# Kernel tuning notes

Measured on AMD Instinct MI355X. Metric: run time of the kernel, lower is better.

Reference implementation:

```python
import jax, jax.numpy as jnp
import numpy as np

N, E = 50000, 800000
NFEAT, NHID, NCLASS = 512, 256, 64
RRELU_SLOPE = (1.0 / 8.0 + 1.0 / 3.0) / 2.0  # nn.RReLU eval-mode negative slope


def spmm(row, col, val, X):
    # sparse adj (COO: row, col, val) @ dense X -> [N, F]
    return jax.ops.segment_sum(X[col] * val[:, None], row, num_segments=N)


def setup_inputs() -> dict:
    key = jax.random.key(0)
    ks = jax.random.split(key, 12)
    x = jax.random.normal(ks[0], (N, NFEAT), dtype=jnp.float32)
    edge_row = jnp.sort(jax.random.randint(ks[1], (E,), 0, N))
    edge_col = jax.random.randint(ks[2], (E,), 0, N)
    # normalized-ish positive adjacency values
    edge_val = jax.random.uniform(ks[3], (E,), dtype=jnp.float32) / 16.0
    def glorot(k, fi, fo):
        s = 1.0 / np.sqrt(fi)
        return jax.random.normal(k, (fi, fo), dtype=jnp.float32) * s
    w1 = glorot(ks[4], NFEAT, NHID)
    b1 = jax.random.normal(ks[5], (NHID,), dtype=jnp.float32) * 0.01
    w2 = glorot(ks[6], NFEAT, NHID)
    b2 = jax.random.normal(ks[7], (NHID,), dtype=jnp.float32) * 0.01
    w3 = glorot(ks[8], NHID, NCLASS)
    b3 = jax.random.normal(ks[9], (NCLASS,), dtype=jnp.float32) * 0.01
    w4 = glorot(ks[10], NFEAT, NCLASS)
    b4 = jax.random.normal(ks[11], (NCLASS,), dtype=jnp.float32) * 0.01
    return {"x": x, "edge_row": edge_row, "edge_col": edge_col, "edge_val": edge_val,
            "w1": w1, "b1": b1, "w2": w2, "b2": b2, "w3": w3, "b3": b3, "w4": w4, "b4": b4}


def reference(x, edge_row, edge_col, edge_val, w1, b1, w2, b2, w3, b3, w4, b4):
    # skip branches (no adj): support = x @ W + b; dropout is identity in eval
    a_skip0 = x @ w2 + b2                                   # [N, NHID]
    a_skip1 = x @ w4 + b4                                   # [N, NCLASS]
    # gc1 with adj
    h1 = spmm(edge_row, edge_col, edge_val, x @ w1) + b1    # [N, NHID]
    v = h1 + a_skip0
    h = jnp.where(v >= 0, v, v * RRELU_SLOPE)               # RReLU (eval mode)
    # gc3 with adj
    out = spmm(edge_row, edge_col, edge_val, h @ w3) + b3 + a_skip1  # [N, NCLASS]
    return (out, w1, w2, w3, w4)
```

## Files before the change

kernel.cpp:

```cpp
#include <hip/hip_runtime.h>

#define N_NODES 50000
#define N_EDGES 800000
#define NFEAT 512
#define NHID 256
#define NCLASS 64
#define NCOMB 576
#define NPAD 640
#define NSKIP 320
#define RRELU_SLOPE 0.2291666666666667f

typedef __attribute__((ext_vector_type(8))) short bf16x8;
typedef __attribute__((ext_vector_type(4))) float f32x4;
typedef __attribute__((ext_vector_type(2))) float f32x2;

#define GLOAD_LDS16(g, l)                                                      \
    __builtin_amdgcn_global_load_lds(                                          \
        (const __attribute__((address_space(1))) void*)(g),                    \
        (__attribute__((address_space(3))) void*)(l), 16, 0, 0)

__device__ __forceinline__ unsigned short f2bf(float f) {
    unsigned int x = __float_as_uint(f);
    unsigned int r = (x + 0x7fffu + ((x >> 16) & 1u)) >> 16;
    return (unsigned short)r;
}
__device__ __forceinline__ float bf2f(unsigned short u) {
    return __uint_as_float(((unsigned int)u) << 16);
}
__device__ __forceinline__ float bf_lo(unsigned int u) { return __uint_as_float(u << 16); }
__device__ __forceinline__ float bf_hi(unsigned int u) { return __uint_as_float(u & 0xffff0000u); }
__device__ __forceinline__ unsigned char f2fp8(float v) {
    return (unsigned char)__builtin_amdgcn_cvt_pk_fp8_f32(v, v, 0, false);
}

#define S0 6400000
#define S1 7200000
#define S2 7527680
#define S3 7577681
#define S4 7594065
#define S5 7594705
#define S6 7672529
#define PREP_BLOCKS ((S6 + 255) / 256)

__global__ __launch_bounds__(256)
void prep(const float* __restrict__ x, const int* __restrict__ erow,
          const int* __restrict__ ecol, const float* __restrict__ ev,
          const float* __restrict__ w1, const float* __restrict__ b1,
          const float* __restrict__ w2, const float* __restrict__ b2,
          const float* __restrict__ w3, const float* __restrict__ b3,
          const float* __restrict__ w4, const float* __restrict__ b4,
          unsigned short* __restrict__ xb, unsigned short* __restrict__ Bt,
          float* __restrict__ biasb, unsigned short* __restrict__ w3t,
          uint2* __restrict__ ep, int* __restrict__ rp,
          float* __restrict__ out) {
    int i = blockIdx.x * 256 + threadIdx.x;
    if (i >= S6) return;
    if (i < S0) {
        float4 v = ((const float4*)x)[i];
        ushort4 o;
        o.x = f2bf(v.x); o.y = f2bf(v.y); o.z = f2bf(v.z); o.w = f2bf(v.w);
        ((ushort4*)xb)[i] = o;
    } else if (i < S1) {
        int j = i - S0;
        uint2 e;
        e.x = (unsigned)ecol[j];
        e.y = __float_as_uint(ev[j]);
        ep[j] = e;
    } else if (i < S2) {
        int j = i - S1;
        int c = j >> 9;
        int k = j & 511;
        float v = 0.f;
        if (c < NHID)            v = w1[k * NHID + c];
        else if (c < 2 * NHID)   v = w2[k * NHID + (c - NHID)];
        else if (c < NCOMB)      v = w4[k * NCLASS + (c - 2 * NHID)];
        Bt[j] = f2bf(v);
    } else if (i < S3) {
        int n = i - S2;
        int lo = 0, hi = N_EDGES;
        while (lo < hi) {
            int mid = (lo + hi) >> 1;
            if (erow[mid] < n) lo = mid + 1; else hi = mid;
        }
        rp[n] = lo;
    } else if (i < S4) {
        int j = i - S3;
        int c = j >> 8;
        int k = j & 255;
        w3t[j] = f2bf(w3[k * NCLASS + c]);
    } else if (i < S5) {
        int b = i - S4;
        float v = 0.f;
        if (b >= NHID && b < 2 * NHID)       v = b1[b - NHID] + b2[b - NHID];
        else if (b >= 2 * NHID && b < NCOMB) v = b3[b - 2 * NHID] + b4[b - 2 * NHID];
        biasb[b] = v;
    } else {
        int j = i - S5;
        float4* o4 = (float4*)out;
        if (j < 32768)        o4[800000 + j] = ((const float4*)w1)[j];
        else if (j < 65536)   o4[832768 + (j - 32768)] = ((const float4*)w2)[j - 32768];
        else if (j < 69632)   o4[865536 + (j - 65536)] = ((const float4*)w3)[j - 65536];
        else                  o4[869632 + (j - 69632)] = ((const float4*)w4)[j - 69632];
    }
}

#define GBM 128
#define GBK 64
#define NCB0 5
#define NRP0 392

template <int BN, int MODE>
__global__ __launch_bounds__(256, 4)
void gemm_bf16(const unsigned short* __restrict__ A,
               const unsigned short* __restrict__ Bt,
               const float* __restrict__ bias,
               unsigned char* __restrict__ C8,
               unsigned short* __restrict__ skipb,
               int M, int K, int NC) {
    constexpr int CF = BN / 32;
    __shared__ unsigned short As[GBM * GBK];
    __shared__ unsigned short Bs[BN * GBK];
    int row0, col0;
    if (MODE == 0) {
        int b = blockIdx.x;
        int g = b / (8 * NCB0);
        int w = b % (8 * NCB0);
        int r = g * 8 + (w & 7);
        int c = w >> 3;
        if (r * GBM >= M) return;
        row0 = r * GBM;
        col0 = c * BN;
    } else {
        col0 = blockIdx.x * BN;
        row0 = blockIdx.y * GBM;
    }
    const int tid  = threadIdx.x;
    const int lane = tid & 63;
    const int wave = tid >> 6;
    const int wr = (wave >> 1) * 64;
    const int wc = (wave & 1) * (BN / 2);
    const int lm = lane & 15;
    const int l4 = lane >> 4;
    const int sw = lm & 7;

    const int sub  = lane >> 3;
    const int slot = lane & 7;
    const int goct = slot ^ sub;

    f32x4 acc[4][CF] = {};

    for (int k0 = 0; k0 < K; k0 += GBK) {
        #pragma unroll
        for (int p = 0; p < 4; ++p) {
            int chunk = wave * 4 + p;
            int gr = row0 + chunk * 8 + sub;
            if (gr > M - 1) gr = M - 1;
            GLOAD_LDS16(A + (size_t)gr * K + k0 + goct * 8, As + chunk * 512);
        }
        #pragma unroll
        for (int p = 0; p < BN / 32; ++p) {
            int chunk = wave * (BN / 32) + p;
            int rb = col0 + chunk * 8 + sub;
            GLOAD_LDS16(Bt + (size_t)rb * K + k0 + goct * 8, Bs + chunk * 512);
        }
        __syncthreads();

        #pragma unroll
        for (int kk8 = 0; kk8 < GBK / 8; kk8 += 4) {
            const int so = ((kk8 + l4) ^ sw) * 8;
            bf16x8 bfr[CF];
            #pragma unroll
            for (int j = 0; j < CF; ++j)
                bfr[j] = *(const bf16x8*)(Bs + (wc + j * 16 + lm) * 64 + so);
            #pragma unroll
            for (int i = 0; i < 4; ++i) {
                bf16x8 af = *(const bf16x8*)(As + (wr + i * 16 + lm) * 64 + so);
                #pragma unroll
                for (int j = 0; j < CF; ++j)
                    acc[i][j] = __builtin_amdgcn_mfma_f32_16x16x32_bf16(af, bfr[j], acc[i][j], 0, 0, 0);
            }
        }
        __syncthreads();
    }

    #pragma unroll
    for (int i = 0; i < 4; ++i) {
        #pragma unroll
        for (int j = 0; j < CF; ++j) {
            int col = col0 + wc + j * 16 + lm;
            float bvv = (MODE == 0) ? bias[col] : 0.f;
            #pragma unroll
            for (int r = 0; r < 4; ++r) {
                int row = row0 + wr + i * 16 + l4 * 4 + r;
                if (row < M) {
                    float v = acc[i][j][r];
                    if (MODE == 0) {
                        if (col < NHID)       C8[(size_t)row * NHID + col] = f2fp8(v);
                        else if (col < NCOMB) skipb[(size_t)row * NSKIP + (col - NHID)] = f2bf(v + bvv);
                    } else {
                        C8[(size_t)row * NC + col] = f2fp8(v);
                    }
                }
            }
        }
    }
}

__global__ __launch_bounds__(256)
void spmm1_rrelu(const int* __restrict__ rp, const uint2* __restrict__ ep,
                 const unsigned char* __restrict__ xw1q,
                 const unsigned short* __restrict__ skipb,
                 unsigned short* __restrict__ hb, int n_nodes) {
    int n = blockIdx.x * 4 + (threadIdx.x >> 6);
    if (n >= n_nodes) return;
    int lane = threadIdx.x & 63;
    int f = lane * 4;
    int lo = rp[n], hi = rp[n + 1];
    float s0 = 0.f, s1 = 0.f, s2 = 0.f, s3 = 0.f;
    int e = lo;
    for (; e + 7 < hi; e += 8) {
        uint2 ed[8];
        unsigned p[8];
        #pragma unroll
        for (int q = 0; q < 8; ++q) ed[q] = ep[e + q];
        #pragma unroll
        for (int q = 0; q < 8; ++q)
            p[q] = *(const unsigned*)(xw1q + (size_t)ed[q].x * NHID + f);
        #pragma unroll
        for (int q = 0; q < 8; ++q) {
            float v = __uint_as_float(ed[q].y);
            f32x2 ab = __builtin_amdgcn_cvt_pk_f32_fp8((int)p[q], false);
            f32x2 cd = __builtin_amdgcn_cvt_pk_f32_fp8((int)p[q], true);
            s0 += v * ab.x;
            s1 += v * ab.y;
            s2 += v * cd.x;
            s3 += v * cd.y;
        }
    }
    for (; e < hi; ++e) {
        uint2 ee = ep[e];
        float v = __uint_as_float(ee.y);
        unsigned p = *(const unsigned*)(xw1q + (size_t)ee.x * NHID + f);
        f32x2 ab = __builtin_amdgcn_cvt_pk_f32_fp8((int)p, false);
        f32x2 cd = __builtin_amdgcn_cvt_pk_f32_fp8((int)p, true);
        s0 += v * ab.x;
        s1 += v * ab.y;
        s2 += v * cd.x;
        s3 += v * cd.y;
    }
    ushort4 sk = *(const ushort4*)(skipb + (size_t)n * NSKIP + f);
    float v0 = s0 + bf2f(sk.x), v1 = s1 + bf2f(sk.y);
    float v2 = s2 + bf2f(sk.z), v3 = s3 + bf2f(sk.w);
    v0 = (v0 >= 0.f) ? v0 : v0 * RRELU_SLOPE;
    v1 = (v1 >= 0.f) ? v1 : v1 * RRELU_SLOPE;
    v2 = (v2 >= 0.f) ? v2 : v2 * RRELU_SLOPE;
    v3 = (v3 >= 0.f) ? v3 : v3 * RRELU_SLOPE;
    ushort4 o;
    o.x = f2bf(v0); o.y = f2bf(v1); o.z = f2bf(v2); o.w = f2bf(v3);
    *(ushort4*)(hb + (size_t)n * NHID + f) = o;
}

__global__ __launch_bounds__(256)
void spmm2_out(const int* __restrict__ rp, const uint2* __restrict__ ep,
               const unsigned char* __restrict__ hw3q,
               const unsigned short* __restrict__ skipb,
               float* __restrict__ out, int n_nodes) {
    int n = blockIdx.x * 4 + (threadIdx.x >> 6);
    if (n >= n_nodes) return;
    int lane = threadIdx.x & 63;
    int q = lane >> 4;
    int l = lane & 15;
    int f = l * 4;
    int lo = rp[n], hi = rp[n + 1];
    float s0 = 0.f, s1 = 0.f, s2 = 0.f, s3 = 0.f;
    int e = lo + q;
    for (; e + 4 < hi; e += 8) {
        uint2 ea = ep[e], eb = ep[e + 4];
        unsigned pa = *(const unsigned*)(hw3q + (size_t)ea.x * NCLASS + f);
        unsigned pb = *(const unsigned*)(hw3q + (size_t)eb.x * NCLASS + f);
        float va = __uint_as_float(ea.y), vb = __uint_as_float(eb.y);
        f32x2 a0 = __builtin_amdgcn_cvt_pk_f32_fp8((int)pa, false);
        f32x2 a1 = __builtin_amdgcn_cvt_pk_f32_fp8((int)pa, true);
        f32x2 b0 = __builtin_amdgcn_cvt_pk_f32_fp8((int)pb, false);
        f32x2 b1 = __builtin_amdgcn_cvt_pk_f32_fp8((int)pb, true);
        s0 += va * a0.x + vb * b0.x;
        s1 += va * a0.y + vb * b0.y;
        s2 += va * a1.x + vb * b1.x;
        s3 += va * a1.y + vb * b1.y;
    }
    for (; e < hi; e += 4) {
        uint2 ee = ep[e];
        unsigned p = *(const unsigned*)(hw3q + (size_t)ee.x * NCLASS + f);
        float v = __uint_as_float(ee.y);
        f32x2 ab = __builtin_amdgcn_cvt_pk_f32_fp8((int)p, false);
        f32x2 cd = __builtin_amdgcn_cvt_pk_f32_fp8((int)p, true);
        s0 += v * ab.x;
        s1 += v * ab.y;
        s2 += v * cd.x;
        s3 += v * cd.y;
    }
    s0 += __shfl_xor(s0, 16); s0 += __shfl_xor(s0, 32);
    s1 += __shfl_xor(s1, 16); s1 += __shfl_xor(s1, 32);
    s2 += __shfl_xor(s2, 16); s2 += __shfl_xor(s2, 32);
    s3 += __shfl_xor(s3, 16); s3 += __shfl_xor(s3, 32);
    if (q == 0) {
        uint2 sv = *(const uint2*)(skipb + (size_t)n * NSKIP + NHID + f);
        float4 o;
        o.x = s0 + bf_lo(sv.x);
        o.y = s1 + bf_hi(sv.x);
        o.z = s2 + bf_lo(sv.y);
        o.w = s3 + bf_hi(sv.y);
        *(float4*)(out + (size_t)n * NCLASS + f) = o;
    }
}

extern "C" void kernel_launch(void* const* d_in, const int* in_sizes, int n_in,
                              void* d_out, int out_size, void* d_ws, size_t ws_size,
                              hipStream_t stream) {
    const float* x    = (const float*)d_in[0];
    const int*   erow = (const int*)d_in[1];
    const int*   ecol = (const int*)d_in[2];
    const float* ev   = (const float*)d_in[3];
    const float* w1   = (const float*)d_in[4];
    const float* b1   = (const float*)d_in[5];
    const float* w2   = (const float*)d_in[6];
    const float* b2   = (const float*)d_in[7];
    const float* w3   = (const float*)d_in[8];
    const float* b3   = (const float*)d_in[9];
    const float* w4   = (const float*)d_in[10];
    const float* b4   = (const float*)d_in[11];
    float* out = (float*)d_out;

    char* ws = (char*)d_ws;
    size_t off = 0;
    auto alloc = [&](size_t bytes) -> void* {
        off = (off + 255) & ~(size_t)255;
        void* p = ws + off;
        off += bytes;
        return p;
    };

    unsigned short* xb    = (unsigned short*)alloc((size_t)N_NODES * NFEAT * 2);
    unsigned short* Bt    = (unsigned short*)alloc((size_t)NFEAT * NPAD * 2);
    float*          biasb = (float*)alloc(NPAD * 4);
    unsigned char*  xw1q  = (unsigned char*)alloc((size_t)N_NODES * NHID);
    unsigned short* skipb = (unsigned short*)alloc((size_t)N_NODES * NSKIP * 2);
    unsigned short* hb    = (unsigned short*)alloc((size_t)N_NODES * NHID * 2);
    unsigned short* w3t   = (unsigned short*)alloc((size_t)NHID * NCLASS * 2);
    unsigned char*  hw3q  = (unsigned char*)alloc((size_t)N_NODES * NCLASS);
    int*            rp    = (int*)alloc((size_t)(N_NODES + 1) * 4);
    uint2*          ep    = (uint2*)alloc((size_t)N_EDGES * 8);

    prep<<<PREP_BLOCKS, 256, 0, stream>>>(x, erow, ecol, ev, w1, b1, w2, b2, w3, b3,
                                          w4, b4, xb, Bt, biasb, w3t, ep, rp, out);

    gemm_bf16<128, 0><<<NRP0 * NCB0, 256, 0, stream>>>(xb, Bt, biasb, xw1q, skipb,
                                                       N_NODES, NFEAT, NPAD);

    spmm1_rrelu<<<(N_NODES + 3) / 4, 256, 0, stream>>>(rp, ep, xw1q, skipb, hb, N_NODES);

    dim3 g2(NCLASS / 64, (N_NODES + GBM - 1) / GBM);
    gemm_bf16<64, 1><<<g2, 256, 0, stream>>>(hb, w3t, nullptr, hw3q, nullptr,
                                             N_NODES, NHID, NCLASS);

    spmm2_out<<<(N_NODES + 3) / 4, 256, 0, stream>>>(rp, ep, hw3q, skipb, out, N_NODES);
}
```

Baseline: 311.5 us.

## Double-buffer LDS tiles in bf16 GEMM and make K a template constant

The GEMM kernel now keeps two LDS buffers for the A and B tiles. It issues the global-to-LDS loads for the next K step before computing on the current one, and drops the trailing barrier, so memory latency can overlap with MFMA work. K becomes a template parameter, which lets the K loop fully unroll. In exchange LDS use doubles (to about 64KB per block in mode 0) and the launch-bounds occupancy hint drops from 4 to 2, which may lower the number of resident waves.

```diff
diff --git a/kernel.cpp b/kernel.cpp
--- a/kernel.cpp
+++ b/kernel.cpp
@@ -109,17 +109,18 @@
 #define NCB0 5
 #define NRP0 392
 
-template <int BN, int MODE>
-__global__ __launch_bounds__(256, 4)
+template <int BN, int MODE, int K>
+__global__ __launch_bounds__(256, 2)
 void gemm_bf16(const unsigned short* __restrict__ A,
                const unsigned short* __restrict__ Bt,
                const float* __restrict__ bias,
                unsigned char* __restrict__ C8,
                unsigned short* __restrict__ skipb,
-               int M, int K, int NC) {
+               int M, int NC) {
     constexpr int CF = BN / 32;
-    __shared__ unsigned short As[GBM * GBK];
-    __shared__ unsigned short Bs[BN * GBK];
+    constexpr int NIT = K / GBK;
+    __shared__ unsigned short As[2][GBM * GBK];
+    __shared__ unsigned short Bs[2][BN * GBK];
     int row0, col0;
     if (MODE == 0) {
         int b = blockIdx.x;
@@ -147,40 +148,47 @@
     const int slot = lane & 7;
     const int goct = slot ^ sub;
 
-    f32x4 acc[4][CF] = {};
-
-    for (int k0 = 0; k0 < K; k0 += GBK) {
+    auto stage = [&](int k0, unsigned short* Asb, unsigned short* Bsb) {
         #pragma unroll
         for (int p = 0; p < 4; ++p) {
             int chunk = wave * 4 + p;
             int gr = row0 + chunk * 8 + sub;
             if (gr > M - 1) gr = M - 1;
-            GLOAD_LDS16(A + (size_t)gr * K + k0 + goct * 8, As + chunk * 512);
+            GLOAD_LDS16(A + (size_t)gr * K + k0 + goct * 8, Asb + chunk * 512);
         }
         #pragma unroll
         for (int p = 0; p < BN / 32; ++p) {
             int chunk = wave * (BN / 32) + p;
             int rb = col0 + chunk * 8 + sub;
-            GLOAD_LDS16(Bt + (size_t)rb * K + k0 + goct * 8, Bs + chunk * 512);
-        }
+            GLOAD_LDS16(Bt + (size_t)rb * K + k0 + goct * 8, Bsb + chunk * 512);
+        }
+    };
+
+    f32x4 acc[4][CF] = {};
+
+    stage(0, As[0], Bs[0]);
+
+    #pragma unroll
+    for (int it = 0; it < NIT; ++it) {
         __syncthreads();
-
+        if (it + 1 < NIT) stage((it + 1) * GBK, As[(it + 1) & 1], Bs[(it + 1) & 1]);
+        const unsigned short* Ac = As[it & 1];
+        const unsigned short* Bc = Bs[it & 1];
         #pragma unroll
         for (int kk8 = 0; kk8 < GBK / 8; kk8 += 4) {
             const int so = ((kk8 + l4) ^ sw) * 8;
             bf16x8 bfr[CF];
             #pragma unroll
             for (int j = 0; j < CF; ++j)
-                bfr[j] = *(const bf16x8*)(Bs + (wc + j * 16 + lm) * 64 + so);
+                bfr[j] = *(const bf16x8*)(Bc + (wc + j * 16 + lm) * 64 + so);
             #pragma unroll
             for (int i = 0; i < 4; ++i) {
-                bf16x8 af = *(const bf16x8*)(As + (wr + i * 16 + lm) * 64 + so);
+                bf16x8 af = *(const bf16x8*)(Ac + (wr + i * 16 + lm) * 64 + so);
                 #pragma unroll
                 for (int j = 0; j < CF; ++j)
                     acc[i][j] = __builtin_amdgcn_mfma_f32_16x16x32_bf16(af, bfr[j], acc[i][j], 0, 0, 0);
             }
         }
-        __syncthreads();
     }
 
     #pragma unroll
@@ -354,14 +362,14 @@
     prep<<<PREP_BLOCKS, 256, 0, stream>>>(x, erow, ecol, ev, w1, b1, w2, b2, w3, b3,
                                           w4, b4, xb, Bt, biasb, w3t, ep, rp, out);
 
-    gemm_bf16<128, 0><<<NRP0 * NCB0, 256, 0, stream>>>(xb, Bt, biasb, xw1q, skipb,
-                                                       N_NODES, NFEAT, NPAD);
+    gemm_bf16<128, 0, NFEAT><<<NRP0 * NCB0, 256, 0, stream>>>(xb, Bt, biasb, xw1q, skipb,
+                                                              N_NODES, NPAD);
 
     spmm1_rrelu<<<(N_NODES + 3) / 4, 256, 0, stream>>>(rp, ep, xw1q, skipb, hb, N_NODES);
 
     dim3 g2(NCLASS / 64, (N_NODES + GBM - 1) / GBM);
-    gemm_bf16<64, 1><<<g2, 256, 0, stream>>>(hb, w3t, nullptr, hw3q, nullptr,
-                                             N_NODES, NHID, NCLASS);
+    gemm_bf16<64, 1, NHID><<<g2, 256, 0, stream>>>(hb, w3t, nullptr, hw3q, nullptr,
+                                                   N_NODES, NCLASS);
 
     spmm2_out<<<(N_NODES + 3) / 4, 256, 0, stream>>>(rp, ep, hw3q, skipb, out, N_NODES);
 }
```

New measurement: 322.2 us. 1.03x slower.
